# Optimization experiments

Measured on AMD Instinct MI355X. Metric: run time of the kernel, lower is better.

## Reference

```python
import jax, jax.numpy as jnp
import numpy as np

B, LQ, LKV, C, H, Z = 4, 1024, 4096, 256, 8, 1024


def setup_inputs() -> dict:
    key = jax.random.key(0)
    ks = jax.random.split(key, 10)
    s = 0.02  # small init scale for weights
    return {
        "q": jax.random.normal(ks[0], (B, LQ, C), jnp.float32),
        "kv": jax.random.normal(ks[1], (B, LKV, C), jnp.float32),
        "q_ape": jax.random.normal(ks[2], (1, LQ, C), jnp.float32),
        "k_ape": jax.random.normal(ks[3], (1, LKV - Z, C), jnp.float32),
        "attn_pos": jax.random.normal(ks[4], (1, H, LQ, Z), jnp.float32),
        "Wq": jax.random.normal(ks[5], (C, C), jnp.float32) * s,
        "Wk": jax.random.normal(ks[6], (C, C), jnp.float32) * s,
        "Wv": jax.random.normal(ks[7], (C, C), jnp.float32) * s,
        "Wp": jax.random.normal(ks[8], (C, C), jnp.float32) * s,
        "bp": jnp.zeros((C,), jnp.float32),
        "z_shape": Z,
    }


def reference(q, kv, q_ape, k_ape, attn_pos, Wq, Wk, Wv, Wp, bp, z_shape):
    Bn, Lq, Cd = q.shape
    d = Cd // H
    scale = d ** (-0.5)
    # q path: APE added before projection
    qh = ((q + q_ape) @ Wq.T).reshape(Bn, Lq, H, d).transpose(0, 2, 1, 3)  # (B,H,Lq,d)
    # in-place `k[:, z_shape:, :] += k_ape` in torch aliases kv, so v also sees it
    kvm = kv.at[:, z_shape:, :].add(k_ape)
    kh = (kvm @ Wk.T).reshape(Bn, -1, H, d).transpose(0, 2, 1, 3)  # (B,H,Lkv,d)
    vh = (kvm @ Wv.T).reshape(Bn, -1, H, d).transpose(0, 2, 1, 3)  # (B,H,Lkv,d)
    attn = jnp.einsum('bhqd,bhkd->bhqk', qh, kh) * scale           # (B,H,Lq,Lkv)
    # partial positional bias on the template slice only
    attn = attn.at[:, :, :, :z_shape].add(attn_pos)
    attn = jax.nn.softmax(attn, axis=-1)
    x = jnp.einsum('bhqk,bhkd->bhqd', attn, vh)
    x = x.transpose(0, 2, 1, 3).reshape(Bn, Lq, Cd)
    return x @ Wp.T + bp
```

## Files before the change

kernel.cpp:

```cpp
#include <hip/hip_runtime.h>


typedef __attribute__((ext_vector_type(8))) short bf16x8;
typedef __attribute__((ext_vector_type(4))) float f32x4;
typedef __attribute__((ext_vector_type(4))) unsigned short u16x4;

#define MFMA16(a, b, c) __builtin_amdgcn_mfma_f32_16x16x32_bf16((a), (b), (c), 0, 0, 0)

__device__ __forceinline__ unsigned short f2bf(float f) {
  return __builtin_bit_cast(unsigned short, static_cast<__bf16>(f));
}
__device__ __forceinline__ float bf2f(unsigned short u) {
  return __builtin_bit_cast(float, ((unsigned)u) << 16);
}

__global__ __launch_bounds__(256) void prep_all(const float* __restrict__ Wq,
                                                const float* __restrict__ Wk,
                                                const float* __restrict__ Wv,
                                                const float* __restrict__ Wp,
                                                const float* __restrict__ pos,
                                                const float* __restrict__ Xq,
                                                const float* __restrict__ Xkv,
                                                const float* __restrict__ q_ape,
                                                const float* __restrict__ k_ape,
                                                unsigned short* __restrict__ wout,
                                                unsigned short* __restrict__ pfb,
                                                unsigned short* __restrict__ kvp,
                                                unsigned short* __restrict__ qp,
                                                int posBlocks) {
  int bx = blockIdx.x;
  if (bx < posBlocks) {
    const int s4 = bx * 256 + threadIdx.x;
    const int zk4 = s4 & 255, q = (s4 >> 8) & 1023, h = s4 >> 18;
    const float4 v = *(const float4*)(pos + ((size_t)s4 << 2));
    const int kt = zk4 >> 4, c = (zk4 >> 2) & 3, g = zk4 & 3;
    const float L = 1.4426950408889634f;
    u16x4 o = { f2bf(v.x * L), f2bf(v.y * L), f2bf(v.z * L), f2bf(v.w * L) };
    *(u16x4*)(pfb + (size_t)((h << 6) + (q >> 4)) * 16384 + ((kt << 2) + c) * 256 + ((q & 15) << 4) + (g << 2)) = o;
    return;
  }
  bx -= posBlocks;
  if (bx < 128) {
    const int idx = bx * 256 + threadIdx.x;
    const int which = idx >> 13, rem = idx & 8191;
    const int o = rem >> 5, colb = (rem & 31) << 3;
    const float* src = (which == 0) ? Wq : (which == 1) ? Wk : (which == 2) ? Wv : Wp;
    float4 v0 = *(const float4*)(src + (size_t)o * 256 + colb);
    float4 v1 = *(const float4*)(src + (size_t)o * 256 + colb + 4);
    if (which == 0) {
      const float qs = 0.17677669529663687f * 1.4426950408889634f;
      v0.x *= qs; v0.y *= qs; v0.z *= qs; v0.w *= qs;
      v1.x *= qs; v1.y *= qs; v1.z *= qs; v1.w *= qs;
    }
    const int n = o >> 4, x = o & 15, k = colb >> 5, g = (colb & 31) >> 3;
    unsigned short* dst = wout + (which << 16) + n * 4096 + k * 512 + x * 32 + g * 8;
    u16x4 a = { f2bf(v0.x), f2bf(v0.y), f2bf(v0.z), f2bf(v0.w) };
    u16x4 b = { f2bf(v1.x), f2bf(v1.y), f2bf(v1.z), f2bf(v1.w) };
    *(u16x4*)dst = a;
    *(u16x4*)(dst + 4) = b;
    return;
  }
  bx -= 128;
  if (bx < 2048) {
    const int idx = bx * 256 + threadIdx.x;
    const int row = idx >> 5, c8 = idx & 31;
    const int col = c8 << 3, lq = row & 4095;
    const float* xp = Xkv + (size_t)row * 256 + col;
    float4 v0 = *(const float4*)xp, v1 = *(const float4*)(xp + 4);
    if (lq >= 1024) {
      const float* ap = k_ape + (size_t)(lq - 1024) * 256 + col;
      const float4 a0 = *(const float4*)ap, a1 = *(const float4*)(ap + 4);
      v0.x += a0.x; v0.y += a0.y; v0.z += a0.z; v0.w += a0.w;
      v1.x += a1.x; v1.y += a1.y; v1.z += a1.z; v1.w += a1.w;
    }
    const int k = c8 >> 2, g = c8 & 3;
    unsigned short* dst = kvp + (size_t)(row >> 4) * 4096 + k * 512 + (row & 15) * 32 + g * 8;
    u16x4 a = { f2bf(v0.x), f2bf(v0.y), f2bf(v0.z), f2bf(v0.w) };
    u16x4 b = { f2bf(v1.x), f2bf(v1.y), f2bf(v1.z), f2bf(v1.w) };
    *(u16x4*)dst = a;
    *(u16x4*)(dst + 4) = b;
    return;
  }
  bx -= 2048;
  {
    const int idx = bx * 256 + threadIdx.x;
    const int row = idx >> 5, c8 = idx & 31;
    const int col = c8 << 3, arow = row & 1023;
    const float* xp = Xq + (size_t)row * 256 + col;
    const float* ap = q_ape + (size_t)arow * 256 + col;
    const float4 v0 = *(const float4*)xp, v1 = *(const float4*)(xp + 4);
    const float4 a0 = *(const float4*)ap, a1 = *(const float4*)(ap + 4);
    const int k = c8 >> 2, g = c8 & 3;
    unsigned short* dst = qp + (size_t)(row >> 4) * 4096 + k * 512 + (row & 15) * 32 + g * 8;
    u16x4 a = { f2bf(v0.x + a0.x), f2bf(v0.y + a0.y), f2bf(v0.z + a0.z), f2bf(v0.w + a0.w) };
    u16x4 b = { f2bf(v1.x + a1.x), f2bf(v1.y + a1.y), f2bf(v1.z + a1.z), f2bf(v1.w + a1.w) };
    *(u16x4*)dst = a;
    *(u16x4*)(dst + 4) = b;
  }
}

__global__ __launch_bounds__(256, 4) void proj_qkv(const unsigned short* __restrict__ kvp,
                                                   const unsigned short* __restrict__ qp,
                                                   const unsigned short* __restrict__ Wqb,
                                                   const unsigned short* __restrict__ Wkb,
                                                   const unsigned short* __restrict__ Wvb,
                                                   unsigned short* __restrict__ Qh,
                                                   unsigned short* __restrict__ Khp,
                                                   unsigned short* __restrict__ Vsp) {
  const int tid = threadIdx.x;
  const int w = tid >> 6, lane = tid & 63, x = lane & 15, g = lane >> 4;
  const int rg = w & 1, nh = w >> 1;
  const int bx = blockIdx.x;
  if (bx < 1024) {
    const bool isV = bx >= 512;
    const int bk = isV ? bx - 512 : bx;
    const int rbase = bk * 32 + rg * 16;
    const unsigned short* ap = kvp + (size_t)(rbase >> 4) * 4096 + x * 32 + g * 8;
    bf16x8 a[8];
#pragma unroll
    for (int k = 0; k < 8; ++k) a[k] = *(const bf16x8*)(ap + k * 512);
    const unsigned short* Wb = isV ? Wvb : Wkb;
    f32x4 acc[8];
#pragma unroll
    for (int n = 0; n < 8; ++n) acc[n] = (f32x4){0.f, 0.f, 0.f, 0.f};
#pragma unroll
    for (int k = 0; k < 8; ++k)
#pragma unroll
      for (int n0 = 0; n0 < 8; ++n0) {
        const bf16x8 bw = *(const bf16x8*)(Wb + (size_t)(nh * 8 + n0) * 4096 + k * 512 + x * 32 + g * 8);
        acc[n0] = MFMA16(a[k], bw, acc[n0]);
      }
    if (!isV) {
      const int b2 = rbase >> 12, kk0 = (rbase & 4095) + g * 4;
#pragma unroll
      for (int n0 = 0; n0 < 8; ++n0) {
        const int n = nh * 8 + n0, hh = n >> 1, dd = ((n & 1) << 4) + x;
        unsigned short* kp = Khp + (size_t)(b2 * 8 + hh) * 131072;
#pragma unroll
        for (int r = 0; r < 4; ++r)
          kp[(size_t)(kk0 + r) * 32 + dd] = f2bf(acc[n0][r]);
      }
    } else {
      const int b2 = rbase >> 12, T = (rbase >> 6) & 63, c0 = (rbase >> 4) & 3;
      const int ks = c0 & 1, ih = (c0 >> 1) << 2;
#pragma unroll
      for (int n0 = 0; n0 < 8; ++n0) {
        const int n = nh * 8 + n0, hh = n >> 1, dh = n & 1;
        u16x4 o = { f2bf(acc[n0][0]), f2bf(acc[n0][1]), f2bf(acc[n0][2]), f2bf(acc[n0][3]) };
        *(u16x4*)(Vsp + (size_t)(b2 * 8 + hh) * 131072 + T * 2048 + ks * 1024 + dh * 512 + g * 128 + x * 8 + ih) = o;
      }
    }
  } else {
    const int bq = bx - 1024;
    const int rbase = bq * 32 + rg * 16;
    const unsigned short* ap = qp + (size_t)(rbase >> 4) * 4096 + x * 32 + g * 8;
    bf16x8 a[8];
#pragma unroll
    for (int k = 0; k < 8; ++k) a[k] = *(const bf16x8*)(ap + k * 512);
    f32x4 acc[8];
#pragma unroll
    for (int n = 0; n < 8; ++n) acc[n] = (f32x4){0.f, 0.f, 0.f, 0.f};
#pragma unroll
    for (int k = 0; k < 8; ++k)
#pragma unroll
      for (int n0 = 0; n0 < 8; ++n0) {
        const bf16x8 bw = *(const bf16x8*)(Wqb + (size_t)(nh * 8 + n0) * 4096 + k * 512 + x * 32 + g * 8);
        acc[n0] = MFMA16(a[k], bw, acc[n0]);
      }
#pragma unroll
    for (int n0 = 0; n0 < 8; ++n0) {
      const int n = nh * 8 + n0;
#pragma unroll
      for (int r = 0; r < 4; ++r)
        Qh[(size_t)(rbase + g * 4 + r) * 256 + n * 16 + x] = f2bf(acc[n0][r]);
    }
  }
}

template <int SPLIT, bool PF>
__global__ __launch_bounds__(256, 4) void
attn_fused(const unsigned short* __restrict__ Qh,
           const unsigned short* __restrict__ Khp,
           const unsigned short* __restrict__ Vsp,
           const void* __restrict__ pos,
           unsigned short* __restrict__ Xo,
           float* __restrict__ Opart,
           float* __restrict__ lpart) {
  const int tid = threadIdx.x;
  const int w = tid >> 6, lane = tid & 63, x = lane & 15, g = lane >> 4;
  const int bid = blockIdx.x;
  const int h = bid & 7, b = (bid >> 3) & 3, qt = (bid >> 5) & 7, z = bid >> 8;
  const int qrow0 = qt * 128 + w * 32;
  const int NT = 64 / SPLIT;

  const bf16x8 aq0 = *(const bf16x8*)(Qh + (size_t)((b << 10) + qrow0 + x) * 256 + h * 32 + g * 8);
  const bf16x8 aq1 = *(const bf16x8*)(Qh + (size_t)((b << 10) + qrow0 + 16 + x) * 256 + h * 32 + g * 8);
  const unsigned short* Kpl = Khp + (size_t)(b * 8 + h) * 131072 + x * 32 + g * 8;
  const unsigned short* Vpl = Vsp + (size_t)(b * 8 + h) * 131072 + g * 128 + x * 8;
  const unsigned short* pq0 = PF ? (const unsigned short*)pos + (size_t)((h << 6) + (qt << 3) + (w << 1)) * 16384 : nullptr;
  const unsigned short* pq1 = PF ? pq0 + 16384 : nullptr;
  const float* pr0 = PF ? nullptr : (const float*)pos + (size_t)((h << 10) + qrow0 + x) * 1024;
  const float* pr1 = PF ? nullptr : (const float*)pos + (size_t)((h << 10) + qrow0 + 16 + x) * 1024;
  const f32x4 zc = {0.f, 0.f, 0.f, 0.f};

  f32x4 o00 = zc, o01 = zc, o10 = zc, o11 = zc;
  float ls0 = 0.f, ls1 = 0.f;

  bf16x8 ka[4], va[4];
#pragma unroll
  for (int c = 0; c < 4; ++c)
    ka[c] = *(const bf16x8*)(Kpl + (size_t)((z << 6) + c * 16) * 32);
#pragma unroll
  for (int j = 0; j < 4; ++j)
    va[j] = *(const bf16x8*)(Vpl + (z << 11) + (j << 9));

#define TILE(T, BIAS)                                                                        \
  do {                                                                                       \
    const int tp = ((T) + SPLIT <= 63) ? (T) + SPLIT : (T);                                  \
    f32x4 s0[4], s1[4];                                                                      \
    _Pragma("unroll")                                                                        \
    for (int c = 0; c < 4; ++c) s0[c] = MFMA16(ka[c], aq0, zc);                              \
    _Pragma("unroll")                                                                        \
    for (int c = 0; c < 4; ++c) s1[c] = MFMA16(ka[c], aq1, zc);                              \
    _Pragma("unroll")                                                                        \
    for (int c = 0; c < 4; ++c)                            \
      ka[c] = *(const bf16x8*)(Kpl + (size_t)((tp << 6) + c * 16) * 32);                     \
    if (BIAS) {                                                                              \
      if (PF) {                                                                              \
        _Pragma("unroll")                                                                    \
        for (int c = 0; c < 4; ++c) {                                                        \
          const u16x4 p0 = *(const u16x4*)(pq0 + ((T) << 10) + (c << 8) + (x << 4) + (g << 2)); \
          const u16x4 p1 = *(const u16x4*)(pq1 + ((T) << 10) + (c << 8) + (x << 4) + (g << 2)); \
          s0[c][0] += bf2f(p0[0]); s0[c][1] += bf2f(p0[1]);                                  \
          s0[c][2] += bf2f(p0[2]); s0[c][3] += bf2f(p0[3]);                                  \
          s1[c][0] += bf2f(p1[0]); s1[c][1] += bf2f(p1[1]);                                  \
          s1[c][2] += bf2f(p1[2]); s1[c][3] += bf2f(p1[3]);                                  \
        }                                                                                    \
      } else {                                                                               \
        const float LOG2E = 1.4426950408889634f;                                             \
        _Pragma("unroll")                                                                    \
        for (int c = 0; c < 4; ++c) {                                                        \
          const float4 p0 = *(const float4*)(pr0 + ((T) << 6) + c * 16 + g * 4);             \
          const float4 p1 = *(const float4*)(pr1 + ((T) << 6) + c * 16 + g * 4);             \
          s0[c][0] = fmaf(p0.x, LOG2E, s0[c][0]); s0[c][1] = fmaf(p0.y, LOG2E, s0[c][1]);    \
          s0[c][2] = fmaf(p0.z, LOG2E, s0[c][2]); s0[c][3] = fmaf(p0.w, LOG2E, s0[c][3]);    \
          s1[c][0] = fmaf(p1.x, LOG2E, s1[c][0]); s1[c][1] = fmaf(p1.y, LOG2E, s1[c][1]);    \
          s1[c][2] = fmaf(p1.z, LOG2E, s1[c][2]); s1[c][3] = fmaf(p1.w, LOG2E, s1[c][3]);    \
        }                                                                                    \
      }                                                                                      \
    }                                                                                        \
    _Pragma("unroll")                                                                        \
    for (int c = 0; c < 4; ++c)                                                              \
      _Pragma("unroll")                                                                      \
      for (int r = 0; r < 4; ++r) {                                                          \
        s0[c][r] = __builtin_amdgcn_exp2f(s0[c][r]); ls0 += s0[c][r];                        \
        s1[c][r] = __builtin_amdgcn_exp2f(s1[c][r]); ls1 += s1[c][r];                        \
      }                                                                                      \
    bf16x8 pa00, pa01, pa10, pa11;                                                           \
    _Pragma("unroll")                                                                        \
    for (int r = 0; r < 4; ++r) {                                                            \
      pa00[r] = (short)f2bf(s0[0][r]); pa00[4 + r] = (short)f2bf(s0[2][r]);                  \
      pa01[r] = (short)f2bf(s0[1][r]); pa01[4 + r] = (short)f2bf(s0[3][r]);                  \
      pa10[r] = (short)f2bf(s1[0][r]); pa10[4 + r] = (short)f2bf(s1[2][r]);                  \
      pa11[r] = (short)f2bf(s1[1][r]); pa11[4 + r] = (short)f2bf(s1[3][r]);                  \
    }                                                                                        \
    o00 = MFMA16(pa00, va[0], o00); o01 = MFMA16(pa00, va[1], o01);                          \
    o00 = MFMA16(pa01, va[2], o00); o01 = MFMA16(pa01, va[3], o01);                          \
    o10 = MFMA16(pa10, va[0], o10); o11 = MFMA16(pa10, va[1], o11);                          \
    o10 = MFMA16(pa11, va[2], o10); o11 = MFMA16(pa11, va[3], o11);                          \
    _Pragma("unroll")                                                                        \
    for (int j = 0; j < 4; ++j)                            \
      va[j] = *(const bf16x8*)(Vpl + (tp << 11) + (j << 9));                                 \
  } while (0)

  const int nb = 16 / SPLIT;
  int t = z;
  for (int i = 0; i < nb; ++i) { TILE(t, true);  t += SPLIT; }
  for (int i = nb; i < NT; ++i) { TILE(t, false); t += SPLIT; }
#undef TILE

  ls0 += __shfl_xor(ls0, 16); ls0 += __shfl_xor(ls0, 32);
  ls1 += __shfl_xor(ls1, 16); ls1 += __shfl_xor(ls1, 32);

  if (SPLIT == 1) {
    const float inv0 = 1.f / ls0, inv1 = 1.f / ls1;
#pragma unroll
    for (int r = 0; r < 4; ++r) {
      const float ir0 = __shfl(inv0, g * 4 + r, 64);
      const float ir1 = __shfl(inv1, g * 4 + r, 64);
      const size_t orow0 = (size_t)((b << 10) + qrow0 + g * 4 + r) * 256 + h * 32;
      const size_t orow1 = (size_t)((b << 10) + qrow0 + 16 + g * 4 + r) * 256 + h * 32;
      Xo[orow0 + x] = f2bf(o00[r] * ir0);
      Xo[orow0 + 16 + x] = f2bf(o01[r] * ir0);
      Xo[orow1 + x] = f2bf(o10[r] * ir1);
      Xo[orow1 + 16 + x] = f2bf(o11[r] * ir1);
    }
  } else {
    if (g == 0) {
      lpart[(size_t)z * 32768 + ((b << 10) + qrow0 + x) * 8 + h] = ls0;
      lpart[(size_t)z * 32768 + ((b << 10) + qrow0 + 16 + x) * 8 + h] = ls1;
    }
#pragma unroll
    for (int r = 0; r < 4; ++r) {
      const size_t orow0 = (size_t)z * 1048576 + (size_t)((b << 10) + qrow0 + g * 4 + r) * 256 + h * 32;
      const size_t orow1 = (size_t)z * 1048576 + (size_t)((b << 10) + qrow0 + 16 + g * 4 + r) * 256 + h * 32;
      Opart[orow0 + x] = o00[r];
      Opart[orow0 + 16 + x] = o01[r];
      Opart[orow1 + x] = o10[r];
      Opart[orow1 + 16 + x] = o11[r];
    }
  }
}

__global__ __launch_bounds__(256) void combine(const float* __restrict__ Opart,
                                               const float* __restrict__ lpart,
                                               unsigned short* __restrict__ Xo, int split) {
  const int idx = blockIdx.x * 256 + threadIdx.x;
  const int row = idx >> 6, c4 = (idx & 63) << 2, h = c4 >> 5;
  float l = 0.f;
  float4 o = {0.f, 0.f, 0.f, 0.f};
  for (int zz = 0; zz < split; ++zz) {
    l += lpart[(size_t)zz * 32768 + row * 8 + h];
    const float4 ov = *(const float4*)(Opart + (size_t)zz * 1048576 + (size_t)row * 256 + c4);
    o.x += ov.x; o.y += ov.y; o.z += ov.z; o.w += ov.w;
  }
  const float inv = 1.f / l;
  u16x4 pk = { f2bf(o.x * inv), f2bf(o.y * inv), f2bf(o.z * inv), f2bf(o.w * inv) };
  *(u16x4*)(Xo + (size_t)row * 256 + c4) = pk;
}

__global__ __launch_bounds__(256) void proj_out(const unsigned short* __restrict__ Xb,
                                                const unsigned short* __restrict__ Wb,
                                                const float* __restrict__ bias,
                                                float* __restrict__ out) {
  const int tid = threadIdx.x;
  const int w = tid >> 6, lane = tid & 63, x = lane & 15, g = lane >> 4;
  const int rbase = blockIdx.x << 4;
  const int cb = w << 6;
  bf16x8 a[8];
#pragma unroll
  for (int k = 0; k < 8; ++k)
    a[k] = *(const bf16x8*)(Xb + (size_t)(rbase + x) * 256 + k * 32 + g * 8);
  f32x4 acc[4];
#pragma unroll
  for (int n = 0; n < 4; ++n) acc[n] = (f32x4){0.f, 0.f, 0.f, 0.f};
#pragma unroll
  for (int k = 0; k < 8; ++k)
#pragma unroll
    for (int n = 0; n < 4; ++n) {
      const bf16x8 bw = *(const bf16x8*)(Wb + (size_t)((w << 2) + n) * 4096 + k * 512 + x * 32 + g * 8);
      acc[n] = MFMA16(a[k], bw, acc[n]);
    }
#pragma unroll
  for (int n = 0; n < 4; ++n) {
    const float bv = bias[cb + n * 16 + x];
#pragma unroll
    for (int r = 0; r < 4; ++r)
      out[(size_t)(rbase + g * 4 + r) * 256 + cb + n * 16 + x] = acc[n][r] + bv;
  }
}

extern "C" void kernel_launch(void* const* d_in, const int* in_sizes, int n_in,
                              void* d_out, int out_size, void* d_ws, size_t ws_size,
                              hipStream_t stream) {
  const float* q        = (const float*)d_in[0];
  const float* kv       = (const float*)d_in[1];
  const float* q_ape    = (const float*)d_in[2];
  const float* k_ape    = (const float*)d_in[3];
  const float* attn_pos = (const float*)d_in[4];
  const float* Wq       = (const float*)d_in[5];
  const float* Wk       = (const float*)d_in[6];
  const float* Wv       = (const float*)d_in[7];
  const float* Wp       = (const float*)d_in[8];
  const float* bp       = (const float*)d_in[9];
  float* out = (float*)d_out;

  unsigned short* wsb = (unsigned short*)d_ws;
  unsigned short* Wqb = wsb;
  unsigned short* Wkb = wsb + 65536;
  unsigned short* Wvb = wsb + 131072;
  unsigned short* Wpb = wsb + 196608;
  unsigned short* Qh  = wsb + 262144;
  unsigned short* Khp = wsb + 1310720;
  unsigned short* Vsp = wsb + 5505024;
  unsigned short* Xws = wsb + 9699328;
  unsigned short* kvp = wsb + 10747904;
  unsigned short* qp  = wsb + 14942208;

  const size_t L0  = 31981568ull;
  const size_t PFB = 16777216ull;
  const size_t PS  = 4325376ull;
  int split; bool havepf;
  if      (ws_size >= L0 + PFB + 8 * PS) { split = 8; havepf = true; }
  else if (ws_size >= L0 + PFB + 4 * PS) { split = 4; havepf = true; }
  else if (ws_size >= L0 + 4 * PS)       { split = 4; havepf = false; }
  else if (ws_size >= L0 + 2 * PS)       { split = 2; havepf = false; }
  else                                   { split = 1; havepf = false; }
  unsigned short* pfb = (unsigned short*)((char*)d_ws + L0);
  float* Opart = (float*)((char*)d_ws + L0 + (havepf ? PFB : 0));
  float* lpart = Opart + (size_t)split * 1048576;

  const int posBlocks = havepf ? 8192 : 0;
  prep_all<<<posBlocks + 128 + 2048 + 512, 256, 0, stream>>>(
      Wq, Wk, Wv, Wp, attn_pos, q, kv, q_ape, k_ape, wsb, pfb, kvp, qp, posBlocks);
  proj_qkv<<<1152, 256, 0, stream>>>(kvp, qp, Wqb, Wkb, Wvb, Qh, Khp, Vsp);
  if (havepf && split == 8)
    attn_fused<8, true><<<2048, 256, 0, stream>>>(Qh, Khp, Vsp, pfb, Xws, Opart, lpart);
  else if (havepf)
    attn_fused<4, true><<<1024, 256, 0, stream>>>(Qh, Khp, Vsp, pfb, Xws, Opart, lpart);
  else if (split == 4)
    attn_fused<4, false><<<1024, 256, 0, stream>>>(Qh, Khp, Vsp, attn_pos, Xws, Opart, lpart);
  else if (split == 2)
    attn_fused<2, false><<<512, 256, 0, stream>>>(Qh, Khp, Vsp, attn_pos, Xws, Opart, lpart);
  else
    attn_fused<1, false><<<256, 256, 0, stream>>>(Qh, Khp, Vsp, attn_pos, Xws, Opart, lpart);
  if (split > 1) combine<<<1024, 256, 0, stream>>>(Opart, lpart, Xws, split);
  proj_out<<<256, 256, 0, stream>>>(Xws, Wpb, bp, out);
}
```

Baseline: 94.45 us.

## Store Q per-head contiguous, split tile into per-row-group passes, drop split 8

The Q projection now writes Q head-major as (b,h,row,32) so each attention block reads a contiguous per-head plane instead of strided 512-byte rows. The attention tile body is restructured into two sequential groups, one per 16-row Q fragment, to lower live registers, and the K/V prefetch for the next tile moves after both groups. The split-8 configuration is removed, so large workspaces now use split 4 with the prefetched bf16 bias. Together these trade parallelism for fewer partial outputs and a smaller combine, and change how loads overlap with MFMA work.

```diff
diff --git a/kernel.cpp b/kernel.cpp
--- a/kernel.cpp
+++ b/kernel.cpp
@@ -104,7 +104,7 @@
                                                    const unsigned short* __restrict__ Wqb,
                                                    const unsigned short* __restrict__ Wkb,
                                                    const unsigned short* __restrict__ Wvb,
-                                                   unsigned short* __restrict__ Qh,
+                                                   unsigned short* __restrict__ Qhp,
                                                    unsigned short* __restrict__ Khp,
                                                    unsigned short* __restrict__ Vsp) {
   const int tid = threadIdx.x;
@@ -167,19 +167,21 @@
         const bf16x8 bw = *(const bf16x8*)(Wqb + (size_t)(nh * 8 + n0) * 4096 + k * 512 + x * 32 + g * 8);
         acc[n0] = MFMA16(a[k], bw, acc[n0]);
       }
+    const int b2 = rbase >> 10, qr0 = (rbase & 1023) + g * 4;
 #pragma unroll
     for (int n0 = 0; n0 < 8; ++n0) {
-      const int n = nh * 8 + n0;
+      const int n = nh * 8 + n0, hh = n >> 1, dd = ((n & 1) << 4) + x;
+      unsigned short* qpn = Qhp + (size_t)(b2 * 8 + hh) * 32768;
 #pragma unroll
       for (int r = 0; r < 4; ++r)
-        Qh[(size_t)(rbase + g * 4 + r) * 256 + n * 16 + x] = f2bf(acc[n0][r]);
+        qpn[(size_t)(qr0 + r) * 32 + dd] = f2bf(acc[n0][r]);
     }
   }
 }
 
 template <int SPLIT, bool PF>
 __global__ __launch_bounds__(256, 4) void
-attn_fused(const unsigned short* __restrict__ Qh,
+attn_fused(const unsigned short* __restrict__ Qhp,
            const unsigned short* __restrict__ Khp,
            const unsigned short* __restrict__ Vsp,
            const void* __restrict__ pos,
@@ -193,8 +195,9 @@
   const int qrow0 = qt * 128 + w * 32;
   const int NT = 64 / SPLIT;
 
-  const bf16x8 aq0 = *(const bf16x8*)(Qh + (size_t)((b << 10) + qrow0 + x) * 256 + h * 32 + g * 8);
-  const bf16x8 aq1 = *(const bf16x8*)(Qh + (size_t)((b << 10) + qrow0 + 16 + x) * 256 + h * 32 + g * 8);
+  const unsigned short* Qpl = Qhp + (size_t)(b * 8 + h) * 32768;
+  const bf16x8 aq0 = *(const bf16x8*)(Qpl + (size_t)(qrow0 + x) * 32 + g * 8);
+  const bf16x8 aq1 = *(const bf16x8*)(Qpl + (size_t)(qrow0 + 16 + x) * 32 + g * 8);
   const unsigned short* Kpl = Khp + (size_t)(b * 8 + h) * 131072 + x * 32 + g * 8;
   const unsigned short* Vpl = Vsp + (size_t)(b * 8 + h) * 131072 + g * 128 + x * 8;
   const unsigned short* pq0 = PF ? (const unsigned short*)pos + (size_t)((h << 6) + (qt << 3) + (w << 1)) * 16384 : nullptr;
@@ -214,38 +217,26 @@
   for (int j = 0; j < 4; ++j)
     va[j] = *(const bf16x8*)(Vpl + (z << 11) + (j << 9));
 
-#define TILE(T, BIAS)                                                                        \
+#define GROUP(AQ, PQ, PR, LS, OA, OB, T, BIAS)                                               \
   do {                                                                                       \
-    const int tp = ((T) + SPLIT <= 63) ? (T) + SPLIT : (T);                                  \
-    f32x4 s0[4], s1[4];                                                                      \
+    f32x4 s[4];                                                                              \
     _Pragma("unroll")                                                                        \
-    for (int c = 0; c < 4; ++c) s0[c] = MFMA16(ka[c], aq0, zc);                              \
-    _Pragma("unroll")                                                                        \
-    for (int c = 0; c < 4; ++c) s1[c] = MFMA16(ka[c], aq1, zc);                              \
-    _Pragma("unroll")                                                                        \
-    for (int c = 0; c < 4; ++c)                            \
-      ka[c] = *(const bf16x8*)(Kpl + (size_t)((tp << 6) + c * 16) * 32);                     \
+    for (int c = 0; c < 4; ++c) s[c] = MFMA16(ka[c], AQ, zc);                                \
     if (BIAS) {                                                                              \
       if (PF) {                                                                              \
         _Pragma("unroll")                                                                    \
         for (int c = 0; c < 4; ++c) {                                                        \
-          const u16x4 p0 = *(const u16x4*)(pq0 + ((T) << 10) + (c << 8) + (x << 4) + (g << 2)); \
-          const u16x4 p1 = *(const u16x4*)(pq1 + ((T) << 10) + (c << 8) + (x << 4) + (g << 2)); \
-          s0[c][0] += bf2f(p0[0]); s0[c][1] += bf2f(p0[1]);                                  \
-          s0[c][2] += bf2f(p0[2]); s0[c][3] += bf2f(p0[3]);                                  \
-          s1[c][0] += bf2f(p1[0]); s1[c][1] += bf2f(p1[1]);                                  \
-          s1[c][2] += bf2f(p1[2]); s1[c][3] += bf2f(p1[3]);                                  \
+          const u16x4 p = *(const u16x4*)(PQ + ((T) << 10) + (c << 8) + (x << 4) + (g << 2)); \
+          s[c][0] += bf2f(p[0]); s[c][1] += bf2f(p[1]);                                      \
+          s[c][2] += bf2f(p[2]); s[c][3] += bf2f(p[3]);                                      \
         }                                                                                    \
       } else {                                                                               \
         const float LOG2E = 1.4426950408889634f;                                             \
         _Pragma("unroll")                                                                    \
         for (int c = 0; c < 4; ++c) {                                                        \
-          const float4 p0 = *(const float4*)(pr0 + ((T) << 6) + c * 16 + g * 4);             \
-          const float4 p1 = *(const float4*)(pr1 + ((T) << 6) + c * 16 + g * 4);             \
-          s0[c][0] = fmaf(p0.x, LOG2E, s0[c][0]); s0[c][1] = fmaf(p0.y, LOG2E, s0[c][1]);    \
-          s0[c][2] = fmaf(p0.z, LOG2E, s0[c][2]); s0[c][3] = fmaf(p0.w, LOG2E, s0[c][3]);    \
-          s1[c][0] = fmaf(p1.x, LOG2E, s1[c][0]); s1[c][1] = fmaf(p1.y, LOG2E, s1[c][1]);    \
-          s1[c][2] = fmaf(p1.z, LOG2E, s1[c][2]); s1[c][3] = fmaf(p1.w, LOG2E, s1[c][3]);    \
+          const float4 p = *(const float4*)(PR + ((T) << 6) + c * 16 + g * 4);               \
+          s[c][0] = fmaf(p.x, LOG2E, s[c][0]); s[c][1] = fmaf(p.y, LOG2E, s[c][1]);          \
+          s[c][2] = fmaf(p.z, LOG2E, s[c][2]); s[c][3] = fmaf(p.w, LOG2E, s[c][3]);          \
         }                                                                                    \
       }                                                                                      \
     }                                                                                        \
@@ -253,21 +244,26 @@
     for (int c = 0; c < 4; ++c)                                                              \
       _Pragma("unroll")                                                                      \
       for (int r = 0; r < 4; ++r) {                                                          \
-        s0[c][r] = __builtin_amdgcn_exp2f(s0[c][r]); ls0 += s0[c][r];                        \
-        s1[c][r] = __builtin_amdgcn_exp2f(s1[c][r]); ls1 += s1[c][r];                        \
+        s[c][r] = __builtin_amdgcn_exp2f(s[c][r]); LS += s[c][r];                            \
       }                                                                                      \
-    bf16x8 pa00, pa01, pa10, pa11;                                                           \
+    bf16x8 pa0, pa1;                                                                         \
     _Pragma("unroll")                                                                        \
     for (int r = 0; r < 4; ++r) {                                                            \
-      pa00[r] = (short)f2bf(s0[0][r]); pa00[4 + r] = (short)f2bf(s0[2][r]);                  \
-      pa01[r] = (short)f2bf(s0[1][r]); pa01[4 + r] = (short)f2bf(s0[3][r]);                  \
-      pa10[r] = (short)f2bf(s1[0][r]); pa10[4 + r] = (short)f2bf(s1[2][r]);                  \
-      pa11[r] = (short)f2bf(s1[1][r]); pa11[4 + r] = (short)f2bf(s1[3][r]);                  \
+      pa0[r] = (short)f2bf(s[0][r]); pa0[4 + r] = (short)f2bf(s[2][r]);                      \
+      pa1[r] = (short)f2bf(s[1][r]); pa1[4 + r] = (short)f2bf(s[3][r]);                      \
     }                                                                                        \
-    o00 = MFMA16(pa00, va[0], o00); o01 = MFMA16(pa00, va[1], o01);                          \
-    o00 = MFMA16(pa01, va[2], o00); o01 = MFMA16(pa01, va[3], o01);                          \
-    o10 = MFMA16(pa10, va[0], o10); o11 = MFMA16(pa10, va[1], o11);                          \
-    o10 = MFMA16(pa11, va[2], o10); o11 = MFMA16(pa11, va[3], o11);                          \
+    OA = MFMA16(pa0, va[0], OA); OB = MFMA16(pa0, va[1], OB);                                \
+    OA = MFMA16(pa1, va[2], OA); OB = MFMA16(pa1, va[3], OB);                                \
+  } while (0)
+
+#define TILE(T, BIAS)                                                                        \
+  do {                                                                                       \
+    const int tp = ((T) + SPLIT <= 63) ? (T) + SPLIT : (T);                                  \
+    GROUP(aq0, pq0, pr0, ls0, o00, o01, T, BIAS);                                            \
+    GROUP(aq1, pq1, pr1, ls1, o10, o11, T, BIAS);                                            \
+    _Pragma("unroll")                                                                        \
+    for (int c = 0; c < 4; ++c)                            \
+      ka[c] = *(const bf16x8*)(Kpl + (size_t)((tp << 6) + c * 16) * 32);                     \
     _Pragma("unroll")                                                                        \
     for (int j = 0; j < 4; ++j)                            \
       va[j] = *(const bf16x8*)(Vpl + (tp << 11) + (j << 9));                                 \
@@ -278,6 +274,7 @@
   for (int i = 0; i < nb; ++i) { TILE(t, true);  t += SPLIT; }
   for (int i = nb; i < NT; ++i) { TILE(t, false); t += SPLIT; }
 #undef TILE
+#undef GROUP
 
   ls0 += __shfl_xor(ls0, 16); ls0 += __shfl_xor(ls0, 32);
   ls1 += __shfl_xor(ls1, 16); ls1 += __shfl_xor(ls1, 32);
@@ -380,7 +377,7 @@
   unsigned short* Wkb = wsb + 65536;
   unsigned short* Wvb = wsb + 131072;
   unsigned short* Wpb = wsb + 196608;
-  unsigned short* Qh  = wsb + 262144;
+  unsigned short* Qhp = wsb + 262144;
   unsigned short* Khp = wsb + 1310720;
   unsigned short* Vsp = wsb + 5505024;
   unsigned short* Xws = wsb + 9699328;
@@ -391,8 +388,7 @@
   const size_t PFB = 16777216ull;
   const size_t PS  = 4325376ull;
   int split; bool havepf;
-  if      (ws_size >= L0 + PFB + 8 * PS) { split = 8; havepf = true; }
-  else if (ws_size >= L0 + PFB + 4 * PS) { split = 4; havepf = true; }
+  if      (ws_size >= L0 + PFB + 4 * PS) { split = 4; havepf = true; }
   else if (ws_size >= L0 + 4 * PS)       { split = 4; havepf = false; }
   else if (ws_size >= L0 + 2 * PS)       { split = 2; havepf = false; }
   else                                   { split = 1; havepf = false; }
@@ -403,17 +399,15 @@
   const int posBlocks = havepf ? 8192 : 0;
   prep_all<<<posBlocks + 128 + 2048 + 512, 256, 0, stream>>>(
       Wq, Wk, Wv, Wp, attn_pos, q, kv, q_ape, k_ape, wsb, pfb, kvp, qp, posBlocks);
-  proj_qkv<<<1152, 256, 0, stream>>>(kvp, qp, Wqb, Wkb, Wvb, Qh, Khp, Vsp);
-  if (havepf && split == 8)
-    attn_fused<8, true><<<2048, 256, 0, stream>>>(Qh, Khp, Vsp, pfb, Xws, Opart, lpart);
-  else if (havepf)
-    attn_fused<4, true><<<1024, 256, 0, stream>>>(Qh, Khp, Vsp, pfb, Xws, Opart, lpart);
+  proj_qkv<<<1152, 256, 0, stream>>>(kvp, qp, Wqb, Wkb, Wvb, Qhp, Khp, Vsp);
+  if (havepf)
+    attn_fused<4, true><<<1024, 256, 0, stream>>>(Qhp, Khp, Vsp, pfb, Xws, Opart, lpart);
   else if (split == 4)
-    attn_fused<4, false><<<1024, 256, 0, stream>>>(Qh, Khp, Vsp, attn_pos, Xws, Opart, lpart);
+    attn_fused<4, false><<<1024, 256, 0, stream>>>(Qhp, Khp, Vsp, attn_pos, Xws, Opart, lpart);
   else if (split == 2)
-    attn_fused<2, false><<<512, 256, 0, stream>>>(Qh, Khp, Vsp, attn_pos, Xws, Opart, lpart);
+    attn_fused<2, false><<<512, 256, 0, stream>>>(Qhp, Khp, Vsp, attn_pos, Xws, Opart, lpart);
   else
-    attn_fused<1, false><<<256, 256, 0, stream>>>(Qh, Khp, Vsp, attn_pos, Xws, Opart, lpart);
+    attn_fused<1, false><<<256, 256, 0, stream>>>(Qhp, Khp, Vsp, attn_pos, Xws, Opart, lpart);
   if (split > 1) combine<<<1024, 256, 0, stream>>>(Opart, lpart, Xws, split);
   proj_out<<<256, 256, 0, stream>>>(Xws, Wpb, bp, out);
 }
```

New measurement: 88.84 us. 5.9% less time.
